# Kernel tuning notes

Hardware: AMD Instinct MI355X
Metric: run time of the kernel (lower is better)

Reference implementation:

```python
import jax, jax.numpy as jnp
import numpy as np

N, D_IN, D_H = 8192, 512, 512


def setup_inputs() -> dict:
    key = jax.random.key(0)
    kH, kWq, kbq, kWk, kbk = jax.random.split(key, 5)
    s_in = 1.0 / np.sqrt(D_IN)
    return {
        "H": jax.random.normal(kH, (N, D_IN), dtype=jnp.float32),
        "Wq": jax.random.normal(kWq, (D_IN, D_H), dtype=jnp.float32) * s_in,
        "bq": jax.random.normal(kbq, (D_H,), dtype=jnp.float32) * 0.01,
        "Wk": jax.random.normal(kWk, (D_IN, D_H), dtype=jnp.float32) * s_in,
        "bk": jax.random.normal(kbk, (D_H,), dtype=jnp.float32) * 0.01,
    }


def reference(H, Wq, bq, Wk, bk):
    # H: [N, T]; Q, K: [N, d_h]
    Q = H @ Wq + bq
    K = H @ Wk + bk
    # A: [N, N] raw scores
    A = Q @ K.T
    n = A.shape[0]
    # torch.where(eye, 0, A): zero out the diagonal BEFORE scale/softmax
    A = A.at[jnp.arange(n), jnp.arange(n)].set(0.0)
    A = A / jnp.sqrt(jnp.asarray(K.shape[-1], A.dtype))
    A = jax.nn.softmax(A, axis=-1)
    # aggregate values (= H itself) and add residual
    return A @ H + H
```

## Files before the change

### kernel.cpp

```cpp
#include <hip/hip_runtime.h>
#include <cstdint>
#include <cstddef>

#define GLOBAL_AS __attribute__((address_space(1)))
#define LDS_AS __attribute__((address_space(3)))

typedef __attribute__((ext_vector_type(8))) short short8;
typedef __attribute__((ext_vector_type(4))) float floatx4;
typedef __attribute__((ext_vector_type(2))) long long2v;
typedef __attribute__((ext_vector_type(4))) int int4v;
typedef __attribute__((ext_vector_type(8))) int int8v;

#if defined(__has_builtin)
#if __has_builtin(__builtin_amdgcn_cvt_pk_fp8_f32)
#define HAVE_HW_FP8 1
#endif
#endif

static __device__ __forceinline__ unsigned short f2bf(float f) {
  uint32_t u = __builtin_bit_cast(uint32_t, f);
  u += 0x7fffu + ((u >> 16) & 1u);
  return (unsigned short)(u >> 16);
}

static __device__ __forceinline__ unsigned char f2fp8(float f) {
#ifdef HAVE_HW_FP8
  float c = fminf(fmaxf(f, -448.f), 448.f);
  return (unsigned char)(__builtin_amdgcn_cvt_pk_fp8_f32(c, 0.f, 0, false) & 0xff);
#else
  unsigned char s = 0;
  if (f < 0.f) { s = 0x80; f = -f; }
  if (f >= 448.f) return s | 0x7e;
  if (f < 0.015625f) { int r = (int)(f * 512.f + 0.5f); return s | (unsigned char)r; }
  uint32_t u = __builtin_bit_cast(uint32_t, f);
  int e = (int)((u >> 23) & 0xff) - 127;
  uint32_t keep = (u >> 20) & 7, rest = u & 0xfffffu;
  if (rest > 0x80000u || (rest == 0x80000u && (keep & 1))) ++keep;
  if (keep == 8) { keep = 0; ++e; }
  if (e > 8) return s | 0x7e;
  return s | (unsigned char)(((e + 7) << 3) | keep);
#endif
}

static __device__ __forceinline__ uint32_t pack4fp8(const float e[4]) {
#ifdef HAVE_HW_FP8
  const uint32_t p01 = (uint32_t)__builtin_amdgcn_cvt_pk_fp8_f32(e[0], e[1], 0, false);
  const uint32_t p23 = (uint32_t)__builtin_amdgcn_cvt_pk_fp8_f32(e[2], e[3], 0, false);
  return (p01 & 0xffffu) | (p23 << 16);
#else
  return (uint32_t)f2fp8(e[0]) | ((uint32_t)f2fp8(e[1]) << 8) |
         ((uint32_t)f2fp8(e[2]) << 16) | ((uint32_t)f2fp8(e[3]) << 24);
#endif
}

static __device__ __forceinline__ uint32_t gather_dword(uint32_t w, int quad, int l15) {
  const int src = quad * 16 + 4 * (l15 & 3);
  const int sh = (l15 >> 2) * 8;
  const uint32_t v0 = (uint32_t)__shfl((int)w, src);
  const uint32_t v1 = (uint32_t)__shfl((int)w, src + 1);
  const uint32_t v2 = (uint32_t)__shfl((int)w, src + 2);
  const uint32_t v3 = (uint32_t)__shfl((int)w, src + 3);
  return ((v0 >> sh) & 0xffu) | (((v1 >> sh) & 0xffu) << 8) |
         (((v2 >> sh) & 0xffu) << 16) | (((v3 >> sh) & 0xffu) << 24);
}

static __device__ __forceinline__ void wait_vm0() {
  __builtin_amdgcn_s_waitcnt(0x0f70);
}

static __device__ __forceinline__ int8v load_frag32(const unsigned char* base, int row, int quad) {
  const int h = row & 7;
  const int c0 = (2 * quad) ^ h;
  const int c1 = (2 * quad + 1) ^ h;
  const int4v lo = *(const int4v*)(base + row * 128 + c0 * 16);
  const int4v hi = *(const int4v*)(base + row * 128 + c1 * 16);
  int8v r;
  r[0] = lo[0]; r[1] = lo[1]; r[2] = lo[2]; r[3] = lo[3];
  r[4] = hi[0]; r[5] = hi[1]; r[6] = hi[2]; r[7] = hi[3];
  return r;
}

static __device__ __forceinline__ floatx4 mx_mfma(int8v a, int8v b, floatx4 c) {
  return __builtin_amdgcn_mfma_scale_f32_16x16x128_f8f6f4(a, b, c, 0, 0, 0, 0x7f, 0, 0x7f);
}

__global__ __launch_bounds__(256) void transpose_h_kernel(
    const float* __restrict__ in, unsigned char* __restrict__ outT8,
    unsigned short* __restrict__ outN, int R, int C) {
  __shared__ float t[64][65];
  const int bc = blockIdx.x * 64;
  const int br = blockIdx.y * 64;
  const int tc = threadIdx.x & 63;
  const int tr = threadIdx.x >> 6;
  for (int r = tr; r < 64; r += 4) {
    const float v = in[(size_t)(br + r) * C + bc + tc];
    t[r][tc] = v;
    outN[(size_t)(br + r) * C + bc + tc] = f2bf(v);
  }
  __syncthreads();
  for (int r = tr; r < 64; r += 4)
    outT8[(size_t)(bc + r) * R + br + tc] = f2fp8(t[tc][r]);
}

__global__ __launch_bounds__(256) void transpose_w_kernel(
    const float* __restrict__ in, unsigned short* __restrict__ outT, int R, int C) {
  __shared__ float t[64][65];
  const int bc = blockIdx.x * 64;
  const int br = blockIdx.y * 64;
  const int tc = threadIdx.x & 63;
  const int tr = threadIdx.x >> 6;
  for (int r = tr; r < 64; r += 4)
    t[r][tc] = in[(size_t)(br + r) * C + bc + tc];
  __syncthreads();
  for (int r = tr; r < 64; r += 4)
    outT[(size_t)(bc + r) * R + br + tc] = f2bf(t[tc][r]);
}

__global__ __launch_bounds__(256) void pack_bias_kernel(
    const float* __restrict__ bq, const float* __restrict__ bk,
    float* __restrict__ bqk) {
  int i = blockIdx.x * 256 + threadIdx.x;
  bqk[i] = (i < 512) ? bq[i] : bk[i - 512];
}

__global__ __launch_bounds__(256, 4) void gemm_proj(
    const unsigned short* __restrict__ A,
    const unsigned short* __restrict__ Bt,
    int Ncols, int K,
    const float* __restrict__ bias,
    unsigned char* __restrict__ C8)
{
  __shared__ unsigned short As[2][128 * 32];
  __shared__ unsigned short Bs[2][128 * 32];

  const int tid  = threadIdx.x;
  const int lane = tid & 63;
  const int wave = tid >> 6;
  const int wr   = (wave >> 1) * 64;
  const int wc   = (wave & 1) * 64;
  const int quad = lane >> 4;
  const int l15  = lane & 15;
  const int bm   = blockIdx.y * 128;
  const int bn   = blockIdx.x * 128;

  const int c0 = tid, c1 = tid + 256;
  const int r0a = c0 >> 2, k0a = (c0 & 3) << 3;
  const int r1a = c1 >> 2, k1a = (c1 & 3) << 3;

  auto stage = [&](int kt, int b) {
    __builtin_amdgcn_global_load_lds(
        (const GLOBAL_AS void*)(A + (size_t)(bm + r0a) * K + kt + k0a),
        (LDS_AS void*)(&As[b][c0 * 8]), 16, 0, 0);
    __builtin_amdgcn_global_load_lds(
        (const GLOBAL_AS void*)(A + (size_t)(bm + r1a) * K + kt + k1a),
        (LDS_AS void*)(&As[b][c1 * 8]), 16, 0, 0);
    __builtin_amdgcn_global_load_lds(
        (const GLOBAL_AS void*)(Bt + (size_t)(bn + r0a) * K + kt + k0a),
        (LDS_AS void*)(&Bs[b][c0 * 8]), 16, 0, 0);
    __builtin_amdgcn_global_load_lds(
        (const GLOBAL_AS void*)(Bt + (size_t)(bn + r1a) * K + kt + k1a),
        (LDS_AS void*)(&Bs[b][c1 * 8]), 16, 0, 0);
  };

  floatx4 acc[4][4];
#pragma unroll
  for (int i = 0; i < 4; ++i)
#pragma unroll
    for (int j = 0; j < 4; ++j)
      acc[i][j] = (floatx4){0.f, 0.f, 0.f, 0.f};

  stage(0, 0);
  const int nIter = K >> 5;
  for (int it = 0; it < nIter; ++it) {
    const int b = it & 1;
    wait_vm0();
    __syncthreads();
    if (it + 1 < nIter) stage((it + 1) << 5, b ^ 1);

    short8 af[4], bfr[4];
#pragma unroll
    for (int i = 0; i < 4; ++i)
      af[i] = *(const short8*)(&As[b][(wr + i * 16 + l15) * 32 + quad * 8]);
#pragma unroll
    for (int j = 0; j < 4; ++j)
      bfr[j] = *(const short8*)(&Bs[b][(wc + j * 16 + l15) * 32 + quad * 8]);
#pragma unroll
    for (int i = 0; i < 4; ++i)
#pragma unroll
      for (int j = 0; j < 4; ++j)
        acc[i][j] = __builtin_amdgcn_mfma_f32_16x16x32_bf16(af[i], bfr[j], acc[i][j], 0, 0, 0);
  }

#pragma unroll
  for (int i = 0; i < 4; ++i) {
    const int rl = bm + wr + i * 16 + quad * 4;
#pragma unroll
    for (int r = 0; r < 4; ++r) {
      const int row = rl + r;
      float e[4];
#pragma unroll
      for (int j = 0; j < 4; ++j)
        e[j] = acc[i][j][r] + bias[bn + wc + j * 16 + l15];
      const uint32_t d = gather_dword(pack4fp8(e), quad, l15);
      *(uint32_t*)(C8 + (size_t)row * Ncols + bn + wc + 4 * l15) = d;
    }
  }
}

__global__ __launch_bounds__(256, 4) void gemm_qk8(
    const unsigned char* __restrict__ A,
    const unsigned char* __restrict__ Bt,
    int Ncols, int K, int lda, int ldb,
    float* __restrict__ lsum,
    int row0,
    unsigned char* __restrict__ P8)
{
  __shared__ unsigned char As[2][128 * 64];
  __shared__ unsigned char Bs[2][128 * 64];

  const int tid  = threadIdx.x;
  const int lane = tid & 63;
  const int wave = tid >> 6;
  const int wr   = (wave >> 1) * 64;
  const int wc   = (wave & 1) * 64;
  const int quad = lane >> 4;
  const int l15  = lane & 15;
  const int bm   = blockIdx.y * 128;
  const int bn   = blockIdx.x * 128;

  const int c0 = tid, c1 = tid + 256;
  const int r0a = c0 >> 2, k0a = (c0 & 3) << 4;
  const int r1a = c1 >> 2, k1a = (c1 & 3) << 4;

  auto stage = [&](int kt, int b) {
    __builtin_amdgcn_global_load_lds(
        (const GLOBAL_AS void*)(A + (size_t)(bm + r0a) * lda + kt + k0a),
        (LDS_AS void*)(&As[b][c0 * 16]), 16, 0, 0);
    __builtin_amdgcn_global_load_lds(
        (const GLOBAL_AS void*)(A + (size_t)(bm + r1a) * lda + kt + k1a),
        (LDS_AS void*)(&As[b][c1 * 16]), 16, 0, 0);
    __builtin_amdgcn_global_load_lds(
        (const GLOBAL_AS void*)(Bt + (size_t)(bn + r0a) * ldb + kt + k0a),
        (LDS_AS void*)(&Bs[b][c0 * 16]), 16, 0, 0);
    __builtin_amdgcn_global_load_lds(
        (const GLOBAL_AS void*)(Bt + (size_t)(bn + r1a) * ldb + kt + k1a),
        (LDS_AS void*)(&Bs[b][c1 * 16]), 16, 0, 0);
  };

  floatx4 acc[4][4];
#pragma unroll
  for (int i = 0; i < 4; ++i)
#pragma unroll
    for (int j = 0; j < 4; ++j)
      acc[i][j] = (floatx4){0.f, 0.f, 0.f, 0.f};

  stage(0, 0);
  const int nIter = K >> 6;
  for (int it = 0; it < nIter; ++it) {
    const int b = it & 1;
    wait_vm0();
    __syncthreads();
    if (it + 1 < nIter) stage((it + 1) << 6, b ^ 1);

    long2v af[4], bfr[4];
#pragma unroll
    for (int i = 0; i < 4; ++i)
      af[i] = *(const long2v*)(&As[b][(wr + i * 16 + l15) * 64 + quad * 16]);
#pragma unroll
    for (int j = 0; j < 4; ++j)
      bfr[j] = *(const long2v*)(&Bs[b][(wc + j * 16 + l15) * 64 + quad * 16]);
#pragma unroll
    for (int i = 0; i < 4; ++i)
#pragma unroll
      for (int j = 0; j < 4; ++j) {
        acc[i][j] = __builtin_amdgcn_mfma_f32_16x16x32_fp8_fp8(af[i].x, bfr[j].x, acc[i][j], 0, 0, 0);
        acc[i][j] = __builtin_amdgcn_mfma_f32_16x16x32_fp8_fp8(af[i].y, bfr[j].y, acc[i][j], 0, 0, 0);
      }
  }

  const float scale = 0.044194173824159216f;
#pragma unroll
  for (int i = 0; i < 4; ++i) {
    const int rl = bm + wr + i * 16 + quad * 4;
#pragma unroll
    for (int r = 0; r < 4; ++r) {
      const int row = rl + r;
      float e[4];
#pragma unroll
      for (int j = 0; j < 4; ++j) {
        const int col = bn + wc + j * 16 + l15;
        const float lg = ((row0 + row) == col) ? 0.f : acc[i][j][r] * scale;
        e[j] = fminf(__expf(lg), 448.f);
      }
      float rsum = (e[0] + e[1]) + (e[2] + e[3]);
      const uint32_t d = gather_dword(pack4fp8(e), quad, l15);
      *(uint32_t*)(P8 + (size_t)row * Ncols + bn + wc + 4 * l15) = d;
      rsum += __shfl_xor(rsum, 1);
      rsum += __shfl_xor(rsum, 2);
      rsum += __shfl_xor(rsum, 4);
      rsum += __shfl_xor(rsum, 8);
      if (l15 == 0) atomicAdd(&lsum[row0 + row], rsum);
    }
  }
}

template <bool DIRECT>
__global__ __launch_bounds__(256, 3) void gemm_pv8(
    const unsigned char* __restrict__ P,
    const unsigned char* __restrict__ Bt,
    int Kchunk,
    const float* __restrict__ lvec,
    const float* __restrict__ Hres,
    int row0,
    float* __restrict__ outp,
    size_t partStride)
{
  __shared__ unsigned char As[2][64 * 128];
  __shared__ unsigned char Bs[2][128 * 128];

  const int tid  = threadIdx.x;
  const int lane = tid & 63;
  const int wave = tid >> 6;
  const int wr   = (wave >> 1) * 32;
  const int wc   = (wave & 1) * 64;
  const int quad = lane >> 4;
  const int l15  = lane & 15;
  const int bm   = blockIdx.y * 64;
  const int bn   = blockIdx.x * 128;
  const int k0   = blockIdx.z * Kchunk;

  float* part = outp + (DIRECT ? 0 : (size_t)blockIdx.z * partStride);

  const int a0 = tid, a1 = tid + 256;
  const int ar0 = a0 >> 3, ac0 = ((a0 & 7) ^ (ar0 & 7)) << 4;
  const int ar1 = a1 >> 3, ac1 = ((a1 & 7) ^ (ar1 & 7)) << 4;
  const int b0 = tid, b1 = tid + 256, b2 = tid + 512, b3 = tid + 768;
  const int br0 = b0 >> 3, bc0 = ((b0 & 7) ^ (br0 & 7)) << 4;
  const int br1 = b1 >> 3, bc1 = ((b1 & 7) ^ (br1 & 7)) << 4;
  const int br2 = b2 >> 3, bc2 = ((b2 & 7) ^ (br2 & 7)) << 4;
  const int br3 = b3 >> 3, bc3 = ((b3 & 7) ^ (br3 & 7)) << 4;

  auto stage = [&](int kt, int b) {
    __builtin_amdgcn_global_load_lds(
        (const GLOBAL_AS void*)(P + (size_t)(bm + ar0) * 8192 + kt + ac0),
        (LDS_AS void*)(&As[b][a0 * 16]), 16, 0, 0);
    __builtin_amdgcn_global_load_lds(
        (const GLOBAL_AS void*)(P + (size_t)(bm + ar1) * 8192 + kt + ac1),
        (LDS_AS void*)(&As[b][a1 * 16]), 16, 0, 0);
    __builtin_amdgcn_global_load_lds(
        (const GLOBAL_AS void*)(Bt + (size_t)(bn + br0) * 8192 + kt + bc0),
        (LDS_AS void*)(&Bs[b][b0 * 16]), 16, 0, 0);
    __builtin_amdgcn_global_load_lds(
        (const GLOBAL_AS void*)(Bt + (size_t)(bn + br1) * 8192 + kt + bc1),
        (LDS_AS void*)(&Bs[b][b1 * 16]), 16, 0, 0);
    __builtin_amdgcn_global_load_lds(
        (const GLOBAL_AS void*)(Bt + (size_t)(bn + br2) * 8192 + kt + bc2),
        (LDS_AS void*)(&Bs[b][b2 * 16]), 16, 0, 0);
    __builtin_amdgcn_global_load_lds(
        (const GLOBAL_AS void*)(Bt + (size_t)(bn + br3) * 8192 + kt + bc3),
        (LDS_AS void*)(&Bs[b][b3 * 16]), 16, 0, 0);
  };

  floatx4 acc[2][4];
#pragma unroll
  for (int i = 0; i < 2; ++i)
#pragma unroll
    for (int j = 0; j < 4; ++j)
      acc[i][j] = (floatx4){0.f, 0.f, 0.f, 0.f};

  stage(k0, 0);
  const int nIter = Kchunk >> 7;
  for (int it = 0; it < nIter; ++it) {
    const int b = it & 1;
    wait_vm0();
    __syncthreads();
    if (it + 1 < nIter) stage(k0 + ((it + 1) << 7), b ^ 1);

    const int8v af0 = load_frag32(As[b], wr + l15, quad);
    const int8v af1 = load_frag32(As[b], wr + 16 + l15, quad);
#pragma unroll
    for (int j = 0; j < 4; ++j) {
      const int8v bf = load_frag32(Bs[b], wc + j * 16 + l15, quad);
      acc[0][j] = mx_mfma(af0, bf, acc[0][j]);
      acc[1][j] = mx_mfma(af1, bf, acc[1][j]);
    }
  }

#pragma unroll
  for (int i = 0; i < 2; ++i) {
    const int rl = bm + wr + i * 16 + quad * 4;
#pragma unroll
    for (int j = 0; j < 4; ++j) {
      const int col = bn + wc + j * 16 + l15;
#pragma unroll
      for (int r = 0; r < 4; ++r) {
        const int row = rl + r;
        const float v = acc[i][j][r];
        if (DIRECT) {
          const int grow = row0 + row;
          part[(size_t)grow * 512 + col] =
              v / lvec[grow] + Hres[(size_t)grow * 512 + col];
        } else {
          part[(size_t)row * 512 + col] = v;
        }
      }
    }
  }
}

__global__ __launch_bounds__(256) void combine_kernel(
    const float* __restrict__ parts, size_t partStride, int S,
    const float* __restrict__ lvec, const float* __restrict__ Hres,
    float* __restrict__ out, int n4) {
  int i = blockIdx.x * 256 + threadIdx.x;
  if (i >= n4) return;
  float4 a = ((const float4*)parts)[i];
  for (int s = 1; s < S; ++s) {
    const float4 b = ((const float4*)(parts + (size_t)s * partStride))[i];
    a.x += b.x; a.y += b.y; a.z += b.z; a.w += b.w;
  }
  const int row = i >> 7;
  const float inv = 1.f / lvec[row];
  const float4 h = ((const float4*)Hres)[i];
  float4 o;
  o.x = a.x * inv + h.x;
  o.y = a.y * inv + h.y;
  o.z = a.z * inv + h.z;
  o.w = a.w * inv + h.w;
  ((float4*)out)[i] = o;
}

extern "C" void kernel_launch(void* const* d_in, const int* in_sizes, int n_in,
                              void* d_out, int out_size, void* d_ws, size_t ws_size,
                              hipStream_t stream) {
  const float* H  = (const float*)d_in[0];
  const float* Wq = (const float*)d_in[1];
  const float* bq = (const float*)d_in[2];
  const float* Wk = (const float*)d_in[3];
  const float* bk = (const float*)d_in[4];
  float* out = (float*)d_out;

  const int N = 8192, D = 512;

  char* ws = (char*)d_ws;
  size_t off = 0;
  auto alloc = [&](size_t bytes) { char* p = ws + off; off += bytes; return p; };
  unsigned short* Hb   = (unsigned short*)alloc((size_t)N * D * 2);
  unsigned char*  HbT8 = (unsigned char*)alloc((size_t)D * N);
  unsigned char*  QK8  = (unsigned char*)alloc((size_t)N * 2 * D);
  unsigned short* BqkT = (unsigned short*)alloc((size_t)2 * D * D * 2);
  float* bqk = (float*)alloc((size_t)2 * D * 4);
  float* l   = (float*)alloc((size_t)N * 4);
  const size_t base = off;
  unsigned char* P8 = (unsigned char*)(ws + base);

  const size_t pBytes = (size_t)N * N;
  const size_t partBytes = (size_t)N * D * 4;
  const size_t partStride = (size_t)N * D;
  const size_t avail = (ws_size > base) ? (ws_size - base) : 0;

  int S = 0;
  if (avail >= pBytes) {
    const size_t extra = avail - pBytes;
    S = (extra >= 2 * partBytes) ? 2 : 1;
  }
  float* parts = (float*)(ws + base + pBytes);

  hipMemsetAsync(l, 0, (size_t)N * 4, stream);
  transpose_h_kernel<<<dim3(D / 64, N / 64), 256, 0, stream>>>(H, HbT8, Hb, N, D);
  transpose_w_kernel<<<dim3(D / 64, D / 64), 256, 0, stream>>>(Wq, BqkT, D, D);
  transpose_w_kernel<<<dim3(D / 64, D / 64), 256, 0, stream>>>(Wk, BqkT + (size_t)D * D, D, D);
  pack_bias_kernel<<<dim3(4), 256, 0, stream>>>(bq, bk, bqk);

  gemm_proj<<<dim3(2 * D / 128, N / 128), 256, 0, stream>>>(
      Hb, BqkT, 2 * D, D, bqk, QK8);

  if (S >= 1) {
    gemm_qk8<<<dim3(N / 128, N / 128), 256, 0, stream>>>(
        QK8, QK8 + D, N, D, 2 * D, 2 * D, l, 0, P8);
    if (S == 1) {
      gemm_pv8<true><<<dim3(D / 128, N / 64, 1), 256, 0, stream>>>(
          P8, HbT8, N, l, H, 0, out, 0);
    } else {
      gemm_pv8<false><<<dim3(D / 128, N / 64, S), 256, 0, stream>>>(
          P8, HbT8, N / S, nullptr, nullptr, 0, parts, partStride);
      combine_kernel<<<dim3((N * D / 4 + 255) / 256), 256, 0, stream>>>(
          parts, partStride, S, l, H, out, N * D / 4);
    }
  } else {
    int maxRows = (int)(avail / (size_t)N);
    maxRows &= ~127;
    if (maxRows < 128) maxRows = 128;
    for (int r0 = 0; r0 < N; r0 += maxRows) {
      int rows = N - r0;
      if (rows > maxRows) rows = maxRows;
      gemm_qk8<<<dim3(N / 128, rows / 128), 256, 0, stream>>>(
          QK8 + (size_t)r0 * 2 * D, QK8 + D, N, D, 2 * D, 2 * D, l, r0, P8);
      gemm_pv8<true><<<dim3(D / 128, rows / 64, 1), 256, 0, stream>>>(
          P8, HbT8, N, l, H, r0, out, 0);
    }
  }
}
```

Measured before the change: 264.8 us.

## Swizzle LDS staging and store permuted fp8 columns to drop epilogue shuffles

```diff
diff --git a/kernel.cpp b/kernel.cpp
--- a/kernel.cpp
+++ b/kernel.cpp
@@ -53,16 +53,6 @@
 #endif
 }
 
-static __device__ __forceinline__ uint32_t gather_dword(uint32_t w, int quad, int l15) {
-  const int src = quad * 16 + 4 * (l15 & 3);
-  const int sh = (l15 >> 2) * 8;
-  const uint32_t v0 = (uint32_t)__shfl((int)w, src);
-  const uint32_t v1 = (uint32_t)__shfl((int)w, src + 1);
-  const uint32_t v2 = (uint32_t)__shfl((int)w, src + 2);
-  const uint32_t v3 = (uint32_t)__shfl((int)w, src + 3);
-  return ((v0 >> sh) & 0xffu) | (((v1 >> sh) & 0xffu) << 8) |
-         (((v2 >> sh) & 0xffu) << 16) | (((v3 >> sh) & 0xffu) << 24);
-}
 
 static __device__ __forceinline__ void wait_vm0() {
   __builtin_amdgcn_s_waitcnt(0x0f70);
@@ -98,8 +88,9 @@
     outN[(size_t)(br + r) * C + bc + tc] = f2bf(v);
   }
   __syncthreads();
+  const int tperm = 4 * (tc & 15) + (tc >> 4);
   for (int r = tr; r < 64; r += 4)
-    outT8[(size_t)(bc + r) * R + br + tc] = f2fp8(t[tc][r]);
+    outT8[(size_t)(bc + r) * R + br + tperm] = f2fp8(t[tc][r]);
 }
 
 __global__ __launch_bounds__(256) void transpose_w_kernel(
@@ -144,8 +135,8 @@
   const int bn   = blockIdx.x * 128;
 
   const int c0 = tid, c1 = tid + 256;
-  const int r0a = c0 >> 2, k0a = (c0 & 3) << 3;
-  const int r1a = c1 >> 2, k1a = (c1 & 3) << 3;
+  const int r0a = c0 >> 2, k0a = (((c0 & 3) ^ ((c0 >> 3) & 3)) << 3);
+  const int r1a = c1 >> 2, k1a = (((c1 & 3) ^ ((c1 >> 3) & 3)) << 3);
 
   auto stage = [&](int kt, int b) {
     __builtin_amdgcn_global_load_lds(
@@ -170,6 +161,7 @@
       acc[i][j] = (floatx4){0.f, 0.f, 0.f, 0.f};
 
   stage(0, 0);
+  const int swq = quad ^ ((l15 >> 1) & 3);
   const int nIter = K >> 5;
   for (int it = 0; it < nIter; ++it) {
     const int b = it & 1;
@@ -180,10 +172,10 @@
     short8 af[4], bfr[4];
 #pragma unroll
     for (int i = 0; i < 4; ++i)
-      af[i] = *(const short8*)(&As[b][(wr + i * 16 + l15) * 32 + quad * 8]);
+      af[i] = *(const short8*)(&As[b][(wr + i * 16 + l15) * 32 + swq * 8]);
 #pragma unroll
     for (int j = 0; j < 4; ++j)
-      bfr[j] = *(const short8*)(&Bs[b][(wc + j * 16 + l15) * 32 + quad * 8]);
+      bfr[j] = *(const short8*)(&Bs[b][(wc + j * 16 + l15) * 32 + swq * 8]);
 #pragma unroll
     for (int i = 0; i < 4; ++i)
 #pragma unroll
@@ -201,7 +193,7 @@
 #pragma unroll
       for (int j = 0; j < 4; ++j)
         e[j] = acc[i][j][r] + bias[bn + wc + j * 16 + l15];
-      const uint32_t d = gather_dword(pack4fp8(e), quad, l15);
+      const uint32_t d = pack4fp8(e);
       *(uint32_t*)(C8 + (size_t)row * Ncols + bn + wc + 4 * l15) = d;
     }
   }
@@ -229,8 +221,8 @@
   const int bn   = blockIdx.x * 128;
 
   const int c0 = tid, c1 = tid + 256;
-  const int r0a = c0 >> 2, k0a = (c0 & 3) << 4;
-  const int r1a = c1 >> 2, k1a = (c1 & 3) << 4;
+  const int r0a = c0 >> 2, k0a = (((c0 & 3) ^ ((c0 >> 3) & 3)) << 4);
+  const int r1a = c1 >> 2, k1a = (((c1 & 3) ^ ((c1 >> 3) & 3)) << 4);
 
   auto stage = [&](int kt, int b) {
     __builtin_amdgcn_global_load_lds(
@@ -255,6 +247,7 @@
       acc[i][j] = (floatx4){0.f, 0.f, 0.f, 0.f};
 
   stage(0, 0);
+  const int swq = quad ^ ((l15 >> 1) & 3);
   const int nIter = K >> 6;
   for (int it = 0; it < nIter; ++it) {
     const int b = it & 1;
@@ -265,10 +258,10 @@
     long2v af[4], bfr[4];
 #pragma unroll
     for (int i = 0; i < 4; ++i)
-      af[i] = *(const long2v*)(&As[b][(wr + i * 16 + l15) * 64 + quad * 16]);
+      af[i] = *(const long2v*)(&As[b][(wr + i * 16 + l15) * 64 + swq * 16]);
 #pragma unroll
     for (int j = 0; j < 4; ++j)
-      bfr[j] = *(const long2v*)(&Bs[b][(wc + j * 16 + l15) * 64 + quad * 16]);
+      bfr[j] = *(const long2v*)(&Bs[b][(wc + j * 16 + l15) * 64 + swq * 16]);
 #pragma unroll
     for (int i = 0; i < 4; ++i)
 #pragma unroll
@@ -293,7 +286,7 @@
         e[j] = fminf(__expf(lg), 448.f);
       }
       float rsum = (e[0] + e[1]) + (e[2] + e[3]);
-      const uint32_t d = gather_dword(pack4fp8(e), quad, l15);
+      const uint32_t d = pack4fp8(e);
       *(uint32_t*)(P8 + (size_t)row * Ncols + bn + wc + 4 * l15) = d;
       rsum += __shfl_xor(rsum, 1);
       rsum += __shfl_xor(rsum, 2);
```

Measured after the change: 257.6 us. 2.7% less time.
